# Optimization experiments

Measured on AMD Instinct MI355X. Metric: run time of the kernel, lower is better.

Reference implementation:

```python
import jax, jax.numpy as jnp
import numpy as np

N_NODES, N_EDGES, D_IN, D_HID, D_OUT = 50000, 800000, 128, 64, 32


def _glorot(key, shape):
    lim = jnp.sqrt(6.0 / (shape[0] + shape[1]))
    return jax.random.uniform(key, shape, minval=-lim, maxval=lim, dtype=jnp.float32)


def setup_inputs() -> dict:
    key = jax.random.key(0)
    ks = jax.random.split(key, 12)
    return {
        "x": jax.random.normal(ks[0], (N_NODES, D_IN), jnp.float32),
        "edge_index": jax.random.randint(ks[1], (2, N_EDGES), 0, N_NODES, dtype=jnp.int64),
        "edge_weight": jax.random.uniform(ks[2], (N_EDGES,), jnp.float32),
        # layer 1: GATv2Conv(D_IN -> D_HID, heads=1, edge_dim=1)
        "Wl1": _glorot(ks[3], (D_HID, D_IN)), "bl1": jnp.zeros((D_HID,), jnp.float32),
        "Wr1": _glorot(ks[4], (D_HID, D_IN)), "br1": jnp.zeros((D_HID,), jnp.float32),
        "We1": _glorot(ks[5], (D_HID, 1)),
        "att1": _glorot(ks[6], (1, D_HID))[0],
        "bias1": jnp.zeros((D_HID,), jnp.float32),
        # layer 2: GATv2Conv(D_HID -> D_OUT, heads=1, edge_dim=1)
        "Wl2": _glorot(ks[7], (D_OUT, D_HID)), "bl2": jnp.zeros((D_OUT,), jnp.float32),
        "Wr2": _glorot(ks[8], (D_OUT, D_HID)), "br2": jnp.zeros((D_OUT,), jnp.float32),
        "We2": _glorot(ks[9], (D_OUT, 1)),
        "att2": _glorot(ks[10], (1, D_OUT))[0],
        "bias2": jnp.zeros((D_OUT,), jnp.float32),
    }


def _segment_softmax(scores, seg, n):
    m = jax.ops.segment_max(scores, seg, num_segments=n)
    e = jnp.exp(scores - m[seg])
    s = jax.ops.segment_sum(e, seg, num_segments=n)
    return e / s[seg]


def _gatv2(x, src, dst, attr, Wl, bl, Wr, br, We, att, bias, n):
    # PyG GATv2Conv, heads=1, share_weights=False
    xl = x @ Wl.T + bl                    # source transform  [N, D]
    xr = x @ Wr.T + br                    # target transform  [N, D]
    ea = attr @ We.T                      # edge-attr embed   [E, D]
    m = jax.nn.leaky_relu(xl[src] + xr[dst] + ea, negative_slope=0.2)
    score = m @ att                       # [E]
    alpha = _segment_softmax(score, dst, n)
    out = jax.ops.segment_sum(alpha[:, None] * xl[src], dst, num_segments=n)
    return out + bias


def _forward(x, edge_index, edge_weight,
             Wl1, bl1, Wr1, br1, We1, att1, bias1,
             Wl2, bl2, Wr2, br2, We2, att2, bias2):
    n = x.shape[0]
    src, dst = edge_index[0], edge_index[1]
    attr = edge_weight[:, None]           # edge_dim = 1
    # PyG add_self_loops (default True) with fill_value='mean':
    # self-loop attr = mean of incoming edge_attr per node (0 if none)
    cnt = jax.ops.segment_sum(jnp.ones_like(edge_weight), dst, num_segments=n)
    loop_attr = jax.ops.segment_sum(attr, dst, num_segments=n) / jnp.maximum(cnt, 1.0)[:, None]
    loop = jnp.arange(n, dtype=src.dtype)
    src2 = jnp.concatenate([src, loop])
    dst2 = jnp.concatenate([dst, loop])
    attr2 = jnp.concatenate([attr, loop_attr], axis=0)
    h = jax.nn.elu(_gatv2(x, src2, dst2, attr2, Wl1, bl1, Wr1, br1, We1, att1, bias1, n))
    z = _gatv2(h, src2, dst2, attr2, Wl2, bl2, Wr2, br2, We2, att2, bias2, n)
    return jax.nn.softplus(z) + 0.0001


def reference(x, edge_index, edge_weight,
              Wl1, bl1, Wr1, br1, We1, att1, bias1,
              Wl2, bl2, Wr2, br2, We2, att2, bias2):
    return _forward(x, edge_index, edge_weight,
                    Wl1, bl1, Wr1, br1, We1, att1, bias1,
                    Wl2, bl2, Wr2, br2, We2, att2, bias2)
```

## Files before the change

### kernel.cpp

```cpp
#include <hip/hip_runtime.h>
#include <math.h>

typedef unsigned short ushort_t;
typedef __attribute__((ext_vector_type(8))) short bf16x8;
typedef __attribute__((ext_vector_type(4))) float f32x4;

template<int CTRL>
__device__ __forceinline__ float dpp_addf(float x)
{
    int y = __builtin_amdgcn_update_dpp(0, __float_as_int(x), CTRL, 0xf, 0xf, true);
    return x + __int_as_float(y);
}

template<int LPE>
__device__ __forceinline__ float group_reduce(float p)
{
    p = dpp_addf<0xB1>(p);
    p = dpp_addf<0x4E>(p);
    if constexpr (LPE >= 8)  p = dpp_addf<0x141>(p);
    if constexpr (LPE >= 16) p = dpp_addf<0x140>(p);
    return p;
}

__device__ __forceinline__ ushort_t f2bf(float f)
{
    unsigned u = __float_as_uint(f);
    return (ushort_t)((u + 0x7fffu + ((u >> 16) & 1u)) >> 16);
}

__global__ __launch_bounds__(256)
void setup_kernel(const float* __restrict__ Wl1, const float* __restrict__ Wr1,
                  const float* __restrict__ Wl2, const float* __restrict__ Wr2,
                  ushort_t* __restrict__ wab1, ushort_t* __restrict__ wab2,
                  int* __restrict__ cnt, int n)
{
    const int T = gridDim.x * 256;
    const int i0 = blockIdx.x * 256 + threadIdx.x;
    for (int k = i0; k < n; k += T) cnt[k] = 0;
    for (int k = i0; k < 2 * 64 * 128; k += T)
        wab1[k] = f2bf(k < 64 * 128 ? Wl1[k] : Wr1[k - 64 * 128]);
    for (int k = i0; k < 2 * 32 * 64; k += T)
        wab2[k] = f2bf(k < 32 * 64 ? Wl2[k] : Wr2[k - 32 * 64]);
}

template<int N, int K>
__global__ __launch_bounds__(256, 2)
void deg_plus_gemm(const int* __restrict__ ei, int* __restrict__ cnt,
                   int* __restrict__ rank, int E, int degBlocks,
                   const float* __restrict__ X, const ushort_t* __restrict__ Wab,
                   const float* __restrict__ ba, const float* __restrict__ bb,
                   ushort_t* __restrict__ OutA, ushort_t* __restrict__ OutB, int M)
{
    constexpr int KC = K / 32;
    constexpr int NT = N / 16;
    __shared__ ushort_t sW[N * K];
    __shared__ ushort_t sX[64 * K];
    const int tid = threadIdx.x;

    if (blockIdx.x < degBlocks) {
        int e = blockIdx.x * 256 + tid;
        if (e < E) rank[e] = atomicAdd(&cnt[ei[E + e]], 1);
        return;
    }

    const int m0 = (blockIdx.x - degBlocks) * 64;

    auto swz = [](int r, int e) {
        return r * K + ((((e >> 3) ^ (r & 7)) << 3) | (e & 7));
    };

    constexpr int WQ8 = N * K / 8;
    for (int q = tid; q < WQ8; q += 256) {
        int nrow = q / (K / 8);
        int e8   = (q % (K / 8)) * 8;
        uint4 v = *(const uint4*)(Wab + (size_t)nrow * K + e8);
        *(uint4*)&sW[swz(nrow, e8)] = v;
    }
    constexpr int XQ = 64 * (K / 4);
    for (int q = tid; q < XQ; q += 256) {
        int r  = q / (K / 4);
        int k4 = (q % (K / 4)) * 4;
        float4 v = make_float4(0.f, 0.f, 0.f, 0.f);
        int gr = m0 + r;
        if (gr < M) v = *(const float4*)(X + (size_t)gr * K + k4);
        short4 h = make_short4((short)f2bf(v.x), (short)f2bf(v.y),
                               (short)f2bf(v.z), (short)f2bf(v.w));
        *(short4*)&sX[swz(r, k4)] = h;
    }
    __syncthreads();

    const int wv   = tid >> 6;
    const int lane = tid & 63;
    const int mrow = lane & 15;
    const int quad = lane >> 4;

    bf16x8 a[KC];
    #pragma unroll
    for (int kc = 0; kc < KC; ++kc)
        a[kc] = *(const bf16x8*)&sX[swz(wv * 16 + mrow, kc * 32 + quad * 8)];

    #pragma unroll
    for (int nt = 0; nt < NT; ++nt) {
        f32x4 acc = {0.f, 0.f, 0.f, 0.f};
        #pragma unroll
        for (int kc = 0; kc < KC; ++kc) {
            bf16x8 bfr = *(const bf16x8*)&sW[swz(nt * 16 + mrow, kc * 32 + quad * 8)];
            acc = __builtin_amdgcn_mfma_f32_16x16x32_bf16(a[kc], bfr, acc, 0, 0, 0);
        }
        const int col = nt * 16 + mrow;
        ushort_t* dst;
        int cc;
        float bv;
        if (col < N / 2) { dst = OutA; cc = col;         bv = ba[cc]; }
        else             { dst = OutB; cc = col - N / 2; bv = bb[cc]; }
        #pragma unroll
        for (int r = 0; r < 4; ++r) {
            int row = m0 + wv * 16 + quad * 4 + r;
            if (row < M)
                dst[(size_t)row * (N / 2) + cc] = f2bf(acc[r] + bv);
        }
    }
}

__global__ __launch_bounds__(256)
void scan_p1(const int* __restrict__ cnt, int* __restrict__ bsums, int n)
{
    __shared__ int s[256];
    const int tid = threadIdx.x;
    int gi = blockIdx.x * 256 + tid;
    s[tid] = (gi < n) ? cnt[gi] : 0;
    __syncthreads();
    #pragma unroll
    for (int off = 128; off >= 1; off >>= 1) {
        if (tid < off) s[tid] += s[tid + off];
        __syncthreads();
    }
    if (tid == 0) bsums[blockIdx.x] = s[0];
}

__global__ __launch_bounds__(256)
void scan_p3(const int* __restrict__ cnt, const int* __restrict__ bsums,
             int* __restrict__ row_off, int n, int nb)
{
    __shared__ int sb[256];
    __shared__ int s[256];
    const int tid = threadIdx.x;

    int bv = (tid < nb) ? bsums[tid] : 0;
    sb[tid] = bv;
    __syncthreads();
    #pragma unroll
    for (int off = 1; off < 256; off <<= 1) {
        int t = (tid >= off) ? sb[tid - off] : 0;
        __syncthreads();
        sb[tid] += t;
        __syncthreads();
    }
    int excl_t = sb[tid] - bv;
    __syncthreads();
    sb[tid] = excl_t;
    __syncthreads();
    const int base = sb[blockIdx.x];

    int gi = blockIdx.x * 256 + tid;
    int c = (gi < n) ? cnt[gi] : 0;
    s[tid] = c;
    __syncthreads();
    #pragma unroll
    for (int off = 1; off < 256; off <<= 1) {
        int t = (tid >= off) ? s[tid - off] : 0;
        __syncthreads();
        s[tid] += t;
        __syncthreads();
    }
    if (gi < n) {
        int excl = base + s[tid] - c;
        row_off[gi] = excl;
        if (gi == n - 1) row_off[n] = excl + c;
    }
}

__global__ __launch_bounds__(256)
void scatter_kernel(const int* __restrict__ ei, const float* __restrict__ ew,
                    const int* __restrict__ row_off, const int* __restrict__ rank,
                    int2* __restrict__ slot, int E)
{
    int e = blockIdx.x * 256 + threadIdx.x;
    if (e >= E) return;
    int d = ei[E + e];
    slot[row_off[d] + rank[e]] = make_int2(ei[e], __float_as_int(ew[e]));
}

template<int N, int K>
__global__ __launch_bounds__(256, 2)
void gemm_xw_mfma(const float* __restrict__ X, const ushort_t* __restrict__ Wab,
                  const float* __restrict__ ba, const float* __restrict__ bb,
                  ushort_t* __restrict__ OutA, ushort_t* __restrict__ OutB, int M)
{
    constexpr int KC = K / 32;
    constexpr int NT = N / 16;
    __shared__ ushort_t sW[N * K];
    __shared__ ushort_t sX[64 * K];
    const int tid = threadIdx.x;
    const int m0  = blockIdx.x * 64;

    auto swz = [](int r, int e) {
        return r * K + ((((e >> 3) ^ (r & 7)) << 3) | (e & 7));
    };

    constexpr int WQ8 = N * K / 8;
    for (int q = tid; q < WQ8; q += 256) {
        int nrow = q / (K / 8);
        int e8   = (q % (K / 8)) * 8;
        uint4 v = *(const uint4*)(Wab + (size_t)nrow * K + e8);
        *(uint4*)&sW[swz(nrow, e8)] = v;
    }
    constexpr int XQ = 64 * (K / 4);
    for (int q = tid; q < XQ; q += 256) {
        int r  = q / (K / 4);
        int k4 = (q % (K / 4)) * 4;
        float4 v = make_float4(0.f, 0.f, 0.f, 0.f);
        int gr = m0 + r;
        if (gr < M) v = *(const float4*)(X + (size_t)gr * K + k4);
        short4 h = make_short4((short)f2bf(v.x), (short)f2bf(v.y),
                               (short)f2bf(v.z), (short)f2bf(v.w));
        *(short4*)&sX[swz(r, k4)] = h;
    }
    __syncthreads();

    const int wv   = tid >> 6;
    const int lane = tid & 63;
    const int mrow = lane & 15;
    const int quad = lane >> 4;

    bf16x8 a[KC];
    #pragma unroll
    for (int kc = 0; kc < KC; ++kc)
        a[kc] = *(const bf16x8*)&sX[swz(wv * 16 + mrow, kc * 32 + quad * 8)];

    #pragma unroll
    for (int nt = 0; nt < NT; ++nt) {
        f32x4 acc = {0.f, 0.f, 0.f, 0.f};
        #pragma unroll
        for (int kc = 0; kc < KC; ++kc) {
            bf16x8 bfr = *(const bf16x8*)&sW[swz(nt * 16 + mrow, kc * 32 + quad * 8)];
            acc = __builtin_amdgcn_mfma_f32_16x16x32_bf16(a[kc], bfr, acc, 0, 0, 0);
        }
        const int col = nt * 16 + mrow;
        ushort_t* dst;
        int cc;
        float bv;
        if (col < N / 2) { dst = OutA; cc = col;         bv = ba[cc]; }
        else             { dst = OutB; cc = col - N / 2; bv = bb[cc]; }
        #pragma unroll
        for (int r = 0; r < 4; ++r) {
            int row = m0 + wv * 16 + quad * 4 + r;
            if (row < M)
                dst[(size_t)row * (N / 2) + cc] = f2bf(acc[r] + bv);
        }
    }
}

template<int D, int ACT>
__global__ __launch_bounds__(256)
void edge_attn(const ushort_t* __restrict__ xl, const ushort_t* __restrict__ xr,
               const float* __restrict__ We, const float* __restrict__ att,
               const float* __restrict__ bias,
               const int* __restrict__ row_off, const int2* __restrict__ slot,
               float* __restrict__ out, int n)
{
    constexpr int LPE = D / 4;
    constexpr int SG  = 64 / LPE;
    const int lane = threadIdx.x & 63;
    const int wid  = threadIdx.x >> 6;
    const int t    = lane % LPE;
    const int g    = lane / LPE;
    const int node = blockIdx.x * 4 + wid;
    if (node >= n) return;

    auto unpack = [](uint2 d) -> float4 {
        float4 r;
        r.x = __uint_as_float(d.x << 16);
        r.y = __uint_as_float(d.x & 0xffff0000u);
        r.z = __uint_as_float(d.y << 16);
        r.w = __uint_as_float(d.y & 0xffff0000u);
        return r;
    };

    const float4 We4   = *(const float4*)(We   + 4 * t);
    const float4 att4  = *(const float4*)(att  + 4 * t);
    const float4 bias4 = *(const float4*)(bias + 4 * t);
    const float4 xr4   = unpack(*(const uint2*)(xr + (size_t)node * D + 4 * t));

    const int start = row_off[node];
    const int end   = row_off[node + 1];
    const int R  = (end - start) / SG;
    const int jt = start + R * SG;
    const bool has_tail = jt < end;

    int2  q[4];
    uint2 xv[4];
    #pragma unroll
    for (int s = 0; s < 4; ++s) {
        if (s < R) {
            q[s]  = slot[start + s * SG + g];
            xv[s] = *(const uint2*)(xl + (size_t)q[s].x * D + 4 * t);
        }
    }
    int2 tq = make_int2(0, 0);
    uint2 tx = make_uint2(0u, 0u);
    if (has_tail) {
        int idx = min(jt + g, end - 1);
        tq = slot[idx];
        tx = *(const uint2*)(xl + (size_t)tq.x * D + 4 * t);
    }
    const uint2 xs = *(const uint2*)(xl + (size_t)node * D + 4 * t);

    float denom = 0.f, wsum = 0.f;
    float4 acc = make_float4(0.f, 0.f, 0.f, 0.f);

    auto body = [&](int2 qe, float4 xvv, bool active) {
        float w = __int_as_float(qe.y);
        float4 v;
        v.x = xvv.x + fmaf(w, We4.x, xr4.x);
        v.y = xvv.y + fmaf(w, We4.y, xr4.y);
        v.z = xvv.z + fmaf(w, We4.z, xr4.z);
        v.w = xvv.w + fmaf(w, We4.w, xr4.w);
        float4 m;
        m.x = fmaxf(v.x, 0.2f * v.x);
        m.y = fmaxf(v.y, 0.2f * v.y);
        m.z = fmaxf(v.z, 0.2f * v.z);
        m.w = fmaxf(v.w, 0.2f * v.w);
        float p = att4.x * m.x + att4.y * m.y + att4.z * m.z + att4.w * m.w;
        p = group_reduce<LPE>(p);
        float e = active ? __expf(p) : 0.f;
        wsum  += active ? w : 0.f;
        denom += e;
        acc.x = fmaf(e, xvv.x, acc.x);
        acc.y = fmaf(e, xvv.y, acc.y);
        acc.z = fmaf(e, xvv.z, acc.z);
        acc.w = fmaf(e, xvv.w, acc.w);
    };

    int b = 0;
    for (; b + 4 <= R; b += 4) {
        #pragma unroll
        for (int s = 0; s < 4; ++s) {
            int2 cq = q[s]; uint2 cx = xv[s];
            int nr = b + 4 + s;
            if (nr < R) {
                q[s]  = slot[start + nr * SG + g];
                xv[s] = *(const uint2*)(xl + (size_t)q[s].x * D + 4 * t);
            }
            body(cq, unpack(cx), true);
        }
    }
    #pragma unroll
    for (int s = 0; s < 4; ++s)
        if (b + s < R) body(q[s], unpack(xv[s]), true);

    if (has_tail)
        body(tq, unpack(tx), (jt + g) < end);

    #pragma unroll
    for (int mask = LPE; mask < 64; mask <<= 1) {
        denom += __shfl_xor(denom, mask);
        wsum  += __shfl_xor(wsum,  mask);
        acc.x += __shfl_xor(acc.x, mask);
        acc.y += __shfl_xor(acc.y, mask);
        acc.z += __shfl_xor(acc.z, mask);
        acc.w += __shfl_xor(acc.w, mask);
    }

    {
        float w = wsum / (float)max(end - start, 1);
        float4 xvs = unpack(xs);
        float4 v;
        v.x = xvs.x + fmaf(w, We4.x, xr4.x);
        v.y = xvs.y + fmaf(w, We4.y, xr4.y);
        v.z = xvs.z + fmaf(w, We4.z, xr4.z);
        v.w = xvs.w + fmaf(w, We4.w, xr4.w);
        float4 m;
        m.x = fmaxf(v.x, 0.2f * v.x);
        m.y = fmaxf(v.y, 0.2f * v.y);
        m.z = fmaxf(v.z, 0.2f * v.z);
        m.w = fmaxf(v.w, 0.2f * v.w);
        float p = att4.x * m.x + att4.y * m.y + att4.z * m.z + att4.w * m.w;
        p = group_reduce<LPE>(p);
        float e = __expf(p);
        denom += e;
        acc.x = fmaf(e, xvs.x, acc.x);
        acc.y = fmaf(e, xvs.y, acc.y);
        acc.z = fmaf(e, xvs.z, acc.z);
        acc.w = fmaf(e, xvs.w, acc.w);
    }

    float4 res;
    res.x = acc.x / denom + bias4.x;
    res.y = acc.y / denom + bias4.y;
    res.z = acc.z / denom + bias4.z;
    res.w = acc.w / denom + bias4.w;
    if (ACT == 0) {
        res.x = fmaxf(res.x, 0.f) + __expf(fminf(res.x, 0.f)) - 1.f;
        res.y = fmaxf(res.y, 0.f) + __expf(fminf(res.y, 0.f)) - 1.f;
        res.z = fmaxf(res.z, 0.f) + __expf(fminf(res.z, 0.f)) - 1.f;
        res.w = fmaxf(res.w, 0.f) + __expf(fminf(res.w, 0.f)) - 1.f;
    } else {
        res.x = fmaxf(res.x, 0.f) + __logf(1.f + __expf(-fabsf(res.x))) + 1e-4f;
        res.y = fmaxf(res.y, 0.f) + __logf(1.f + __expf(-fabsf(res.y))) + 1e-4f;
        res.z = fmaxf(res.z, 0.f) + __logf(1.f + __expf(-fabsf(res.z))) + 1e-4f;
        res.w = fmaxf(res.w, 0.f) + __logf(1.f + __expf(-fabsf(res.w))) + 1e-4f;
    }
    if (g == 0)
        *(float4*)(out + (size_t)node * D + 4 * t) = res;
}

extern "C" void kernel_launch(void* const* d_in, const int* in_sizes, int n_in,
                              void* d_out, int out_size, void* d_ws, size_t ws_size,
                              hipStream_t stream)
{
    const float* x     = (const float*)d_in[0];
    const int*   ei    = (const int*)d_in[1];
    const float* ew    = (const float*)d_in[2];
    const float* Wl1   = (const float*)d_in[3];
    const float* bl1   = (const float*)d_in[4];
    const float* Wr1   = (const float*)d_in[5];
    const float* br1   = (const float*)d_in[6];
    const float* We1   = (const float*)d_in[7];
    const float* att1  = (const float*)d_in[8];
    const float* bias1 = (const float*)d_in[9];
    const float* Wl2   = (const float*)d_in[10];
    const float* bl2   = (const float*)d_in[11];
    const float* Wr2   = (const float*)d_in[12];
    const float* br2   = (const float*)d_in[13];
    const float* We2   = (const float*)d_in[14];
    const float* att2  = (const float*)d_in[15];
    const float* bias2 = (const float*)d_in[16];
    float* out = (float*)d_out;

    const int n = in_sizes[0] / 128;
    const int E = in_sizes[2];
    const int NB = (n + 255) / 256;
    const int degBlocks  = (E + 255) / 256;
    const int gemmBlocks = (n + 63) / 64;

    char* wp = (char*)d_ws;
    auto carve = [&](size_t bytes) -> void* {
        void* p = (void*)wp;
        wp += (bytes + 255) & ~(size_t)255;
        return p;
    };
    int*      cnt     = (int*)     carve((size_t)n * 4);
    int*      row_off = (int*)     carve((size_t)(n + 1) * 4);
    int*      rank    = (int*)     carve((size_t)E * 4);
    int*      bsums   = (int*)     carve((size_t)256 * 4);
    int2*     slot    = (int2*)    carve((size_t)E * 8);
    ushort_t* wab1    = (ushort_t*)carve((size_t)2 * 64 * 128 * 2);
    ushort_t* wab2    = (ushort_t*)carve((size_t)2 * 32 * 64 * 2);
    ushort_t* xl1     = (ushort_t*)carve((size_t)n * 64 * 2);
    ushort_t* xr1     = (ushort_t*)carve((size_t)n * 64 * 2);
    float*    hbuf    = (float*)   carve((size_t)n * 64 * 4);
    ushort_t* xl2     = (ushort_t*)carve((size_t)n * 32 * 2);
    ushort_t* xr2     = (ushort_t*)carve((size_t)n * 32 * 2);

    setup_kernel<<<256, 256, 0, stream>>>(Wl1, Wr1, Wl2, Wr2, wab1, wab2, cnt, n);

    deg_plus_gemm<128, 128><<<degBlocks + gemmBlocks, 256, 0, stream>>>(
        ei, cnt, rank, E, degBlocks, x, wab1, bl1, br1, xl1, xr1, n);

    scan_p1       <<<NB, 256, 0, stream>>>(cnt, bsums, n);
    scan_p3       <<<NB, 256, 0, stream>>>(cnt, bsums, row_off, n, NB);
    scatter_kernel<<<(E + 255) / 256, 256, 0, stream>>>(ei, ew, row_off, rank, slot, E);

    edge_attn<64, 0><<<(n + 3) / 4, 256, 0, stream>>>(xl1, xr1, We1, att1, bias1,
                                                      row_off, slot, hbuf, n);
    gemm_xw_mfma<64, 64><<<(n + 63) / 64, 256, 0, stream>>>(hbuf, wab2, bl2, br2,
                                                            xl2, xr2, n);
    edge_attn<32, 1><<<(n + 3) / 4, 256, 0, stream>>>(xl2, xr2, We2, att2, bias2,
                                                      row_off, slot, out, n);
}
```

Measured before the change: 252.6 us.

## Replace global atomic degree counting with per-block LDS histograms and column scan

Edge destination counting moves from global atomics into per-block shared-memory histograms, using two packed 16-bit counters per word. Those histograms are written to a block-by-node matrix, which is then column-scanned to give per-block offsets. The scatter into CSR slots is fused with the layer-1 GEMM in place of the degree pass, so the deg_plus_gemm overlap now pairs scatter with GEMM. This is meant to cut contended global atomic traffic. In exchange it adds a 128×n histogram write/read, a column-scan pass, and a hard shared-memory limit on node count (MAXNH).

```diff
diff --git a/kernel.cpp b/kernel.cpp
--- a/kernel.cpp
+++ b/kernel.cpp
@@ -4,6 +4,9 @@
 typedef unsigned short ushort_t;
 typedef __attribute__((ext_vector_type(8))) short bf16x8;
 typedef __attribute__((ext_vector_type(4))) float f32x4;
+
+#define NBLK  128
+#define MAXNH 25024
 
 template<int CTRL>
 __device__ __forceinline__ float dpp_addf(float x)
@@ -31,25 +34,135 @@
 __global__ __launch_bounds__(256)
 void setup_kernel(const float* __restrict__ Wl1, const float* __restrict__ Wr1,
                   const float* __restrict__ Wl2, const float* __restrict__ Wr2,
-                  ushort_t* __restrict__ wab1, ushort_t* __restrict__ wab2,
-                  int* __restrict__ cnt, int n)
+                  ushort_t* __restrict__ wab1, ushort_t* __restrict__ wab2)
 {
     const int T = gridDim.x * 256;
     const int i0 = blockIdx.x * 256 + threadIdx.x;
-    for (int k = i0; k < n; k += T) cnt[k] = 0;
     for (int k = i0; k < 2 * 64 * 128; k += T)
         wab1[k] = f2bf(k < 64 * 128 ? Wl1[k] : Wr1[k - 64 * 128]);
     for (int k = i0; k < 2 * 32 * 64; k += T)
         wab2[k] = f2bf(k < 32 * 64 ? Wl2[k] : Wr2[k - 32 * 64]);
 }
 
+__global__ __launch_bounds__(256, 1)
+void count_hist(const int* __restrict__ ei, ushort_t* __restrict__ lrank,
+                ushort_t* __restrict__ histG, int E, int n, int EPB)
+{
+    __shared__ unsigned h[MAXNH];
+    const int tid = threadIdx.x;
+    const int b   = blockIdx.x;
+    const int nh  = (n + 1) >> 1;
+    for (int i = tid; i < nh; i += 256) h[i] = 0u;
+    __syncthreads();
+
+    const int e0 = b * EPB;
+    const int e1 = min(e0 + EPB, E);
+    for (int e = e0 + tid; e < e1; e += 256) {
+        int d = ei[E + e];
+        unsigned sh  = (unsigned)(d & 1) * 16u;
+        unsigned old = atomicAdd(&h[d >> 1], 1u << sh);
+        lrank[e] = (ushort_t)((old >> sh) & 0xffffu);
+    }
+    __syncthreads();
+
+    ushort_t* row = histG + (size_t)b * n;
+    for (int i = tid; i < n; i += 256) {
+        unsigned v = h[i >> 1];
+        row[i] = (ushort_t)((v >> ((i & 1) * 16)) & 0xffffu);
+    }
+}
+
+__global__ __launch_bounds__(256)
+void col_scan(ushort_t* __restrict__ histG, int* __restrict__ cnt, int n)
+{
+    int idx = blockIdx.x * 256 + threadIdx.x;
+    if (idx >= n) return;
+    unsigned acc = 0;
+    #pragma unroll 1
+    for (int b0 = 0; b0 < NBLK; b0 += 16) {
+        ushort_t c[16];
+        #pragma unroll
+        for (int j = 0; j < 16; ++j)
+            c[j] = histG[(size_t)(b0 + j) * n + idx];
+        #pragma unroll
+        for (int j = 0; j < 16; ++j) {
+            unsigned cc = c[j];
+            histG[(size_t)(b0 + j) * n + idx] = (ushort_t)acc;
+            acc += cc;
+        }
+    }
+    cnt[idx] = (int)acc;
+}
+
+__global__ __launch_bounds__(256)
+void scan_p1(const int* __restrict__ cnt, int* __restrict__ bsums, int n)
+{
+    __shared__ int s[256];
+    const int tid = threadIdx.x;
+    int gi = blockIdx.x * 256 + tid;
+    s[tid] = (gi < n) ? cnt[gi] : 0;
+    __syncthreads();
+    #pragma unroll
+    for (int off = 128; off >= 1; off >>= 1) {
+        if (tid < off) s[tid] += s[tid + off];
+        __syncthreads();
+    }
+    if (tid == 0) bsums[blockIdx.x] = s[0];
+}
+
+__global__ __launch_bounds__(256)
+void scan_p3(const int* __restrict__ cnt, const int* __restrict__ bsums,
+             int* __restrict__ row_off, int n, int nb)
+{
+    __shared__ int sb[256];
+    __shared__ int s[256];
+    const int tid = threadIdx.x;
+
+    int bv = (tid < nb) ? bsums[tid] : 0;
+    sb[tid] = bv;
+    __syncthreads();
+    #pragma unroll
+    for (int off = 1; off < 256; off <<= 1) {
+        int t = (tid >= off) ? sb[tid - off] : 0;
+        __syncthreads();
+        sb[tid] += t;
+        __syncthreads();
+    }
+    int excl_t = sb[tid] - bv;
+    __syncthreads();
+    sb[tid] = excl_t;
+    __syncthreads();
+    const int base = sb[blockIdx.x];
+
+    int gi = blockIdx.x * 256 + tid;
+    int c = (gi < n) ? cnt[gi] : 0;
+    s[tid] = c;
+    __syncthreads();
+    #pragma unroll
+    for (int off = 1; off < 256; off <<= 1) {
+        int t = (tid >= off) ? s[tid - off] : 0;
+        __syncthreads();
+        s[tid] += t;
+        __syncthreads();
+    }
+    if (gi < n) {
+        int excl = base + s[tid] - c;
+        row_off[gi] = excl;
+        if (gi == n - 1) row_off[n] = excl + c;
+    }
+}
+
 template<int N, int K>
 __global__ __launch_bounds__(256, 2)
-void deg_plus_gemm(const int* __restrict__ ei, int* __restrict__ cnt,
-                   int* __restrict__ rank, int E, int degBlocks,
-                   const float* __restrict__ X, const ushort_t* __restrict__ Wab,
-                   const float* __restrict__ ba, const float* __restrict__ bb,
-                   ushort_t* __restrict__ OutA, ushort_t* __restrict__ OutB, int M)
+void scat_plus_gemm(const int* __restrict__ ei, const float* __restrict__ ew,
+                    const int* __restrict__ row_off,
+                    const ushort_t* __restrict__ lrank,
+                    const ushort_t* __restrict__ boff,
+                    int2* __restrict__ slot,
+                    int E, int n, int EPB, int scatBlocks,
+                    const float* __restrict__ X, const ushort_t* __restrict__ Wab,
+                    const float* __restrict__ ba, const float* __restrict__ bb,
+                    ushort_t* __restrict__ OutA, ushort_t* __restrict__ OutB, int M)
 {
     constexpr int KC = K / 32;
     constexpr int NT = N / 16;
@@ -57,13 +170,23 @@
     __shared__ ushort_t sX[64 * K];
     const int tid = threadIdx.x;
 
-    if (blockIdx.x < degBlocks) {
-        int e = blockIdx.x * 256 + tid;
-        if (e < E) rank[e] = atomicAdd(&cnt[ei[E + e]], 1);
+    if (blockIdx.x < scatBlocks) {
+        const int base = blockIdx.x * (256 * 8);
+        #pragma unroll
+        for (int k = 0; k < 8; ++k) {
+            int e = base + k * 256 + tid;
+            if (e < E) {
+                int d  = ei[E + e];
+                int hb = e / EPB;
+                int pos = row_off[d] + (int)boff[(size_t)hb * n + d]
+                                     + (int)lrank[e];
+                slot[pos] = make_int2(ei[e], __float_as_int(ew[e]));
+            }
+        }
         return;
     }
 
-    const int m0 = (blockIdx.x - degBlocks) * 64;
+    const int m0 = (blockIdx.x - scatBlocks) * 64;
 
     auto swz = [](int r, int e) {
         return r * K + ((((e >> 3) ^ (r & 7)) << 3) | (e & 7));
@@ -120,75 +243,6 @@
                 dst[(size_t)row * (N / 2) + cc] = f2bf(acc[r] + bv);
         }
     }
-}
-
-__global__ __launch_bounds__(256)
-void scan_p1(const int* __restrict__ cnt, int* __restrict__ bsums, int n)
-{
-    __shared__ int s[256];
-    const int tid = threadIdx.x;
-    int gi = blockIdx.x * 256 + tid;
-    s[tid] = (gi < n) ? cnt[gi] : 0;
-    __syncthreads();
-    #pragma unroll
-    for (int off = 128; off >= 1; off >>= 1) {
-        if (tid < off) s[tid] += s[tid + off];
-        __syncthreads();
-    }
-    if (tid == 0) bsums[blockIdx.x] = s[0];
-}
-
-__global__ __launch_bounds__(256)
-void scan_p3(const int* __restrict__ cnt, const int* __restrict__ bsums,
-             int* __restrict__ row_off, int n, int nb)
-{
-    __shared__ int sb[256];
-    __shared__ int s[256];
-    const int tid = threadIdx.x;
-
-    int bv = (tid < nb) ? bsums[tid] : 0;
-    sb[tid] = bv;
-    __syncthreads();
-    #pragma unroll
-    for (int off = 1; off < 256; off <<= 1) {
-        int t = (tid >= off) ? sb[tid - off] : 0;
-        __syncthreads();
-        sb[tid] += t;
-        __syncthreads();
-    }
-    int excl_t = sb[tid] - bv;
-    __syncthreads();
-    sb[tid] = excl_t;
-    __syncthreads();
-    const int base = sb[blockIdx.x];
-
-    int gi = blockIdx.x * 256 + tid;
-    int c = (gi < n) ? cnt[gi] : 0;
-    s[tid] = c;
-    __syncthreads();
-    #pragma unroll
-    for (int off = 1; off < 256; off <<= 1) {
-        int t = (tid >= off) ? s[tid - off] : 0;
-        __syncthreads();
-        s[tid] += t;
-        __syncthreads();
-    }
-    if (gi < n) {
-        int excl = base + s[tid] - c;
-        row_off[gi] = excl;
-        if (gi == n - 1) row_off[n] = excl + c;
-    }
-}
-
-__global__ __launch_bounds__(256)
-void scatter_kernel(const int* __restrict__ ei, const float* __restrict__ ew,
-                    const int* __restrict__ row_off, const int* __restrict__ rank,
-                    int2* __restrict__ slot, int E)
-{
-    int e = blockIdx.x * 256 + threadIdx.x;
-    if (e >= E) return;
-    int d = ei[E + e];
-    slot[row_off[d] + rank[e]] = make_int2(ei[e], __float_as_int(ew[e]));
 }
 
 template<int N, int K>
@@ -441,7 +495,8 @@
     const int n = in_sizes[0] / 128;
     const int E = in_sizes[2];
     const int NB = (n + 255) / 256;
-    const int degBlocks  = (E + 255) / 256;
+    const int EPB = (E + NBLK - 1) / NBLK;
+    const int scatBlocks = (E + 2047) / 2048;
     const int gemmBlocks = (n + 63) / 64;
 
     char* wp = (char*)d_ws;
@@ -452,7 +507,8 @@
     };
     int*      cnt     = (int*)     carve((size_t)n * 4);
     int*      row_off = (int*)     carve((size_t)(n + 1) * 4);
-    int*      rank    = (int*)     carve((size_t)E * 4);
+    ushort_t* lrank   = (ushort_t*)carve((size_t)E * 2);
+    ushort_t* histG   = (ushort_t*)carve((size_t)NBLK * n * 2);
     int*      bsums   = (int*)     carve((size_t)256 * 4);
     int2*     slot    = (int2*)    carve((size_t)E * 8);
     ushort_t* wab1    = (ushort_t*)carve((size_t)2 * 64 * 128 * 2);
@@ -463,14 +519,16 @@
     ushort_t* xl2     = (ushort_t*)carve((size_t)n * 32 * 2);
     ushort_t* xr2     = (ushort_t*)carve((size_t)n * 32 * 2);
 
-    setup_kernel<<<256, 256, 0, stream>>>(Wl1, Wr1, Wl2, Wr2, wab1, wab2, cnt, n);
-
-    deg_plus_gemm<128, 128><<<degBlocks + gemmBlocks, 256, 0, stream>>>(
-        ei, cnt, rank, E, degBlocks, x, wab1, bl1, br1, xl1, xr1, n);
-
-    scan_p1       <<<NB, 256, 0, stream>>>(cnt, bsums, n);
-    scan_p3       <<<NB, 256, 0, stream>>>(cnt, bsums, row_off, n, NB);
-    scatter_kernel<<<(E + 255) / 256, 256, 0, stream>>>(ei, ew, row_off, rank, slot, E);
+    setup_kernel<<<256, 256, 0, stream>>>(Wl1, Wr1, Wl2, Wr2, wab1, wab2);
+
+    count_hist<<<NBLK, 256, 0, stream>>>(ei, lrank, histG, E, n, EPB);
+    col_scan  <<<NB, 256, 0, stream>>>(histG, cnt, n);
+    scan_p1   <<<NB, 256, 0, stream>>>(cnt, bsums, n);
+    scan_p3   <<<NB, 256, 0, stream>>>(cnt, bsums, row_off, n, NB);
+
+    scat_plus_gemm<128, 128><<<scatBlocks + gemmBlocks, 256, 0, stream>>>(
+        ei, ew, row_off, lrank, histG, slot, E, n, EPB, scatBlocks,
+        x, wab1, bl1, br1, xl1, xr1, n);
 
     edge_attn<64, 0><<<(n + 3) / 4, 256, 0, stream>>>(xl1, xr1, We1, att1, bias1,
                                                       row_off, slot, hbuf, n);
```

Result: faster. 244.0 us (-3.4%).
